# Kernel optimization log

Hardware: AMD Instinct MI355X
Metric: run time of the kernel (lower is better)

Reference implementation:

```python
import jax, jax.numpy as jnp
import numpy as np

NUM_HEADS = 16
LN_EPS = 1e-5


def _transpose_qkv(X, num_heads):
    # Faithful to the repo's (buggy) transpose_qkv:
    # (B,S,D) -> (B,S,H,D/H) -> permute (B,H,S,D/H) -> reshape (B,S,D)
    B, S, D = X.shape
    X = X.reshape(B, S, num_heads, D // num_heads)
    X = jnp.transpose(X, (0, 2, 1, 3))
    return X.reshape(B, S, D)


def _layer_norm(x, w, b):
    mu = jnp.mean(x, axis=-1, keepdims=True)
    var = jnp.var(x, axis=-1, keepdims=True)
    return (x - mu) * jax.lax.rsqrt(var + LN_EPS) * w + b


def setup_inputs() -> dict:
    key = jax.random.key(0)
    ks = jax.random.split(key, 4)
    B, S, D = 4, 2048, 1024
    scale = 1.0 / np.sqrt(D)
    return {
        "src": jax.random.normal(ks[0], (B, S, D), dtype=jnp.float32),
        "W_q": jax.random.normal(ks[1], (D, D), dtype=jnp.float32) * scale,
        "W_k": jax.random.normal(ks[2], (D, D), dtype=jnp.float32) * scale,
        "W_v": jax.random.normal(ks[3], (D, D), dtype=jnp.float32) * scale,
        "ln1_w": jnp.ones((D,), dtype=jnp.float32),
        "ln1_b": jnp.zeros((D,), dtype=jnp.float32),
        "ln2_w": jnp.ones((D,), dtype=jnp.float32),
        "ln2_b": jnp.zeros((D,), dtype=jnp.float32),
    }


def reference(src, W_q, W_k, W_v, ln1_w, ln1_b, ln2_w, ln2_b):
    # W_* stored as (in, out): y = x @ W  (equivalent to torch Linear, bias=False)
    q = _transpose_qkv(src @ W_q, NUM_HEADS)  # (B,S,D)
    k = _transpose_qkv(src @ W_k, NUM_HEADS)
    v = _transpose_qkv(src @ W_v, NUM_HEADS)
    d = q.shape[-1]  # note: full hidden dim, per the buggy transpose_qkv
    scores = jnp.einsum("bqd,bkd->bqk", q, k) / jnp.sqrt(jnp.float32(d))
    a = jax.nn.softmax(scores, axis=-1)          # (B,S,S) attention weights
    att = jnp.einsum("bqk,bkd->bqd", a, v)       # (B,S,D)
    src2 = _layer_norm(att, ln1_w, ln1_b)        # norm1
    X = _layer_norm(src + src2, ln2_w, ln2_b)    # AddNorm (dropout=0 in eval)
    return (X, a)
```

## Files before the change

### kernel.cpp

```cpp
#include <hip/hip_runtime.h>

typedef _Float16 f16;
typedef __attribute__((ext_vector_type(2))) _Float16 f16x2;
typedef __attribute__((ext_vector_type(4))) _Float16 f16x4;
typedef __attribute__((ext_vector_type(8))) _Float16 f16x8;
typedef __attribute__((ext_vector_type(4))) float f32x4;

#define D_MODEL 1024
#define SEQ 2048
#define NBATCH 4
#define NROWS (NBATCH * SEQ)

__device__ __forceinline__ void gload16(const void* g, void* l) {
  __builtin_amdgcn_global_load_lds(
      (__attribute__((address_space(1))) void*)(void*)g,
      (__attribute__((address_space(3))) void*)l, 16, 0, 0);
}

#define BARF                                   \
  do {                                         \
    asm volatile("" ::: "memory");             \
    __builtin_amdgcn_s_barrier();              \
    asm volatile("" ::: "memory");             \
  } while (0)
#define LGK asm volatile("s_waitcnt lgkmcnt(0)" ::: "memory")
#define LGK8 asm volatile("s_waitcnt lgkmcnt(8)" ::: "memory")
#define PRIO1 __builtin_amdgcn_s_setprio(1)
#define PRIO0 __builtin_amdgcn_s_setprio(0)


#define STAGE_A(D, H)                                        \
  {                                                          \
    f16* d_ = lds + ((D) * 2 + (H)) * 8192 + t * 8;          \
    gload16((H) ? aP2 : aP0, d_);                            \
    gload16((H) ? aP3 : aP1, d_ + 4096);                     \
  }
#define STAGE_B(D, H)                                        \
  {                                                          \
    if constexpr (BN == 256) {                               \
      f16* d_ = lds + 32768 + ((D) * 2 + (H)) * 8192 + t * 8;\
      gload16((H) ? bP2 : bP0, d_);                          \
      gload16((H) ? bP3 : bP1, d_ + 4096);                   \
    } else {                                                 \
      f16* d_ = lds + 32768 + (D) * 8192 + t * 8;            \
      gload16(bP0, d_);                                      \
      gload16(bP1, d_ + 4096);                               \
    }                                                        \
  }
#define ADVA                                                 \
  {                                                          \
    if (ka < NT - 1) {                                       \
      ka++;                                                  \
      aP0 += stepA; aP1 += stepA; aP2 += stepA; aP3 += stepA;\
    }                                                        \
  }
#define ADVB                                                 \
  {                                                          \
    if (kb < NT - 1) {                                       \
      kb++;                                                  \
      bP0 += stepB; bP1 += stepB;                            \
      if constexpr (BN == 256) { bP2 += stepB; bP3 += stepB; } \
    }                                                        \
  }
#define VMC_STEADY                                           \
  {                                                          \
    if constexpr (BN == 256) {                               \
      asm volatile("s_waitcnt vmcnt(4)" ::: "memory");       \
    } else {                                                 \
      asm volatile("s_waitcnt vmcnt(2)" ::: "memory");       \
    }                                                        \
  }
#define RD_A(D, MH)                                          \
  _Pragma("unroll") for (int mi = 0; mi < 4; ++mi)           \
  _Pragma("unroll") for (int kh = 0; kh < 2; ++kh) {         \
    const int rr = (MH) * 64 + mi * 16 + fr;                 \
    fa[mi][kh] = *(const f16x8*)(lds + ((D) * 2 + wm) * 8192 \
        + rr * 64 + (((g0 + kh * 4) ^ (rr & 7)) << 3));      \
  }
#define RD_B(D, NH)                                          \
  _Pragma("unroll") for (int j = 0; j < NJ; ++j)             \
  _Pragma("unroll") for (int kh = 0; kh < 2; ++kh) {         \
    int rbr, base;                                           \
    if constexpr (BN == 256) {                               \
      rbr = (wn & 1) * 64 + fr * 4 + (NH) * 2 + j;           \
      base = 32768 + ((D) * 2 + (wn >> 1)) * 8192;           \
    } else {                                                 \
      rbr = wn * 32 + fr * 2 + (NH);                         \
      base = 32768 + (D) * 8192;                             \
    }                                                        \
    fb[NH][j][kh] = *(const f16x8*)(lds + base + rbr * 64 +  \
        (((g0 + kh * 4) ^ ((rbr >> 2) & 7)) << 3));          \
  }
#define MFMA_Q(MH, NH)                                       \
  _Pragma("unroll") for (int mi = 0; mi < 4; ++mi)           \
  _Pragma("unroll") for (int j = 0; j < NJ; ++j)             \
  _Pragma("unroll") for (int kh = 0; kh < 2; ++kh)           \
    acc[((MH) * 4 + mi) * 2 * NJ + (NH) * NJ + j] =          \
        __builtin_amdgcn_mfma_f32_16x16x32_f16(              \
            fa[mi][kh], fb[NH][j][kh],                       \
            acc[((MH) * 4 + mi) * 2 * NJ + (NH) * NJ + j], 0, 0, 0);

template <int BN>
__device__ __forceinline__ void gemm8p(
    const f16* aP0, const f16* aP1, const f16* aP2, const f16* aP3,
    const f16* bP0, const f16* bP1, const f16* bP2, const f16* bP3,
    int stepA, int stepB, int NT, f16* lds, f32x4* acc)
{
  constexpr int NJ = BN / 128;
  const int t = threadIdx.x, l = t & 63;
  const int w = t >> 6, wm = w >> 2, wn = w & 3;
  const int fr = l & 15, g0 = l >> 4;
  f16x8 fa[4][2], fb[2][NJ][2];
#pragma unroll
  for (int i = 0; i < 8 * 2 * NJ; ++i) acc[i] = f32x4{0.f, 0.f, 0.f, 0.f};
  int ka = 0, kb = 0;
  (void)bP2; (void)bP3;

  STAGE_A(0, 0); STAGE_A(0, 1); ADVA;
  if constexpr (BN == 256) { STAGE_B(0, 0); STAGE_B(0, 1); }
  else { STAGE_B(0, 0); }
  ADVB;
  if constexpr (BN == 256) { STAGE_B(1, 0); STAGE_B(1, 1); }
  else { STAGE_B(1, 0); }
  ADVB;
  VMC_STEADY;
  BARF;

#pragma unroll 1
  for (int it = 0; it < NT / 2; ++it) {
    RD_A(0, 0); RD_B(0, 0);
    STAGE_A(1, 0);
    LGK8;
    BARF; LGK;
    PRIO1; MFMA_Q(0, 0); PRIO0;
    BARF;
    RD_B(0, 1);
    STAGE_A(1, 1); ADVA;
    BARF; LGK;
    PRIO1; MFMA_Q(0, 1); PRIO0;
    BARF;
    RD_A(0, 1);
    STAGE_B(0, 0);
    if constexpr (BN == 128) ADVB;
    BARF; LGK;
    PRIO1; MFMA_Q(1, 0); PRIO0;
    BARF;
    if constexpr (BN == 256) { STAGE_B(0, 1); ADVB; }
    VMC_STEADY;
    BARF;
    PRIO1; MFMA_Q(1, 1); PRIO0;
    BARF;
    RD_A(1, 0); RD_B(1, 0);
    STAGE_A(0, 0);
    LGK8;
    BARF; LGK;
    PRIO1; MFMA_Q(0, 0); PRIO0;
    BARF;
    RD_B(1, 1);
    STAGE_A(0, 1); ADVA;
    BARF; LGK;
    PRIO1; MFMA_Q(0, 1); PRIO0;
    BARF;
    RD_A(1, 1);
    STAGE_B(1, 0);
    if constexpr (BN == 128) ADVB;
    BARF; LGK;
    PRIO1; MFMA_Q(1, 0); PRIO0;
    BARF;
    if constexpr (BN == 256) { STAGE_B(1, 1); ADVB; }
    VMC_STEADY;
    BARF;
    PRIO1; MFMA_Q(1, 1); PRIO0;
    BARF;
  }
}

__global__ __launch_bounds__(512, 2) void k_qkv3(
    const f16* __restrict__ srch, const f16* __restrict__ wt,
    f16* __restrict__ qp, f16* __restrict__ kp, f16* __restrict__ vp)
{
  __shared__ f16 lds[65536];
  const int t = threadIdx.x, l = t & 63;
  const int w = t >> 6, wm = w >> 2, wn = w & 3;
  const int fr = l & 15, g0 = l >> 4, c = t & 7;
  const int bid = blockIdx.x;
  const int sb = (bid & 7) * 48 + (bid >> 3);
  const int bx = sb & 31, by = sb >> 5;
  const int z = by >> 2, cb = by & 3;
  const f16 *aP[4], *bP[4];
#pragma unroll
  for (int i = 0; i < 4; ++i) {
    const int rl = i * 64 + (t >> 3);
    aP[i] = srch + (size_t)(bx * 256 + rl) * 1024 + ((c ^ (rl & 7)) << 3);
    bP[i] = wt + ((size_t)z << 20) + (size_t)(cb * 256 + rl) * 1024 +
            ((c ^ ((rl >> 2) & 7)) << 3);
  }
  f32x4 acc[32];
  gemm8p<256>(aP[0], aP[1], aP[2], aP[3], bP[0], bP[1], bP[2], bP[3],
              64, 64, 16, lds, acc);
  f16* dst = (z == 0) ? qp : (z == 1 ? kp : vp);
  const int col = cb * 256 + wn * 64 + fr * 4;
#pragma unroll
  for (int mi = 0; mi < 8; ++mi)
#pragma unroll
    for (int q = 0; q < 4; ++q) {
      const int row = bx * 256 + wm * 128 + mi * 16 + g0 * 4 + q;
      f16x4 o = {(f16)acc[mi * 4 + 0][q], (f16)acc[mi * 4 + 1][q],
                 (f16)acc[mi * 4 + 2][q], (f16)acc[mi * 4 + 3][q]};
      *(f16x4*)(dst + (size_t)row * 1024 + col) = o;
    }
}

__global__ __launch_bounds__(512, 2) void k_scores(
    const f16* __restrict__ qp, const f16* __restrict__ kp,
    f16* __restrict__ abf)
{
  __shared__ f16 lds[65536];
  const int t = threadIdx.x, l = t & 63;
  const int w = t >> 6, wm = w >> 2, wn = w & 3;
  const int fr = l & 15, g0 = l >> 4, c = t & 7;
  const int b = blockIdx.z;
  const f16* qb = qp + ((size_t)b << 21);
  const f16* kb = kp + ((size_t)b << 21);
  const f16 *aP[4], *bP[4];
#pragma unroll
  for (int i = 0; i < 4; ++i) {
    const int rl = i * 64 + (t >> 3);
    const int spA = blockIdx.x * 256 + rl;
    aP[i] = qb + (size_t)((spA & 127) << 4) * 1024 + ((spA >> 7) << 6) +
            ((c ^ (rl & 7)) << 3);
    const int spB = blockIdx.y * 256 + rl;
    bP[i] = kb + (size_t)((spB & 127) << 4) * 1024 + ((spB >> 7) << 6) +
            ((c ^ ((rl >> 2) & 7)) << 3);
  }
  f32x4 acc[32];
  gemm8p<256>(aP[0], aP[1], aP[2], aP[3], bP[0], bP[1], bP[2], bP[3],
              1024, 1024, 16, lds, acc);
  f16* Cb = abf + ((size_t)b << 22);
  const int col = blockIdx.y * 256 + wn * 64 + fr * 4;
#pragma unroll
  for (int mi = 0; mi < 8; ++mi)
#pragma unroll
    for (int q = 0; q < 4; ++q) {
      const int row = blockIdx.x * 256 + wm * 128 + mi * 16 + g0 * 4 + q;
      f16x4 o = {(f16)(acc[mi * 4 + 0][q] * 0.03125f),
                 (f16)(acc[mi * 4 + 1][q] * 0.03125f),
                 (f16)(acc[mi * 4 + 2][q] * 0.03125f),
                 (f16)(acc[mi * 4 + 3][q] * 0.03125f)};
      *(f16x4*)(Cb + (size_t)row * 2048 + col) = o;
    }
}

__global__ __launch_bounds__(512, 2) void k_att(
    const f16* __restrict__ abf, const f16* __restrict__ vtT,
    f16* __restrict__ attb)
{
  __shared__ f16 lds[49152];
  const int t = threadIdx.x, l = t & 63;
  const int w = t >> 6, wm = w >> 2, wn = w & 3;
  const int fr = l & 15, g0 = l >> 4, c = t & 7;
  const int b = blockIdx.z;
  const f16* ab = abf + ((size_t)b << 22);
  const f16* vb = vtT + ((size_t)b << 21);
  const f16 *aP[4], *bP[2];
#pragma unroll
  for (int i = 0; i < 4; ++i) {
    const int rl = i * 64 + (t >> 3);
    aP[i] = ab + (size_t)(blockIdx.x * 256 + rl) * 2048 + ((c ^ (rl & 7)) << 3);
  }
#pragma unroll
  for (int i = 0; i < 2; ++i) {
    const int rl = i * 64 + (t >> 3);
    bP[i] = vb + (size_t)(blockIdx.y * 128 + rl) * 2048 +
            ((c ^ ((rl >> 2) & 7)) << 3);
  }
  f32x4 acc[16];
  gemm8p<128>(aP[0], aP[1], aP[2], aP[3], bP[0], bP[1], bP[0], bP[0],
              64, 64, 32, lds, acc);
  f16* Cb = attb + ((size_t)b << 21);
  const int col = blockIdx.y * 128 + wn * 32 + fr * 2;
#pragma unroll
  for (int mi = 0; mi < 8; ++mi)
#pragma unroll
    for (int q = 0; q < 4; ++q) {
      const int row = blockIdx.x * 256 + wm * 128 + mi * 16 + g0 * 4 + q;
      f16x2 o = {(f16)acc[mi * 2 + 0][q], (f16)acc[mi * 2 + 1][q]};
      *(f16x2*)(Cb + (size_t)row * 1024 + col) = o;
    }
}

__global__ __launch_bounds__(256) void k_prep(
    const float* __restrict__ src, const float* __restrict__ w0,
    const float* __restrict__ w1, const float* __restrict__ w2,
    f16* __restrict__ srch, f16* __restrict__ wt)
{
  const int b = blockIdx.x, t = threadIdx.x;
  if (b < 4096) {
    const size_t i = (size_t)b * 256 + t;
    const float4* p = (const float4*)src;
    float4 v0 = p[2 * i], v1 = p[2 * i + 1];
    f16x8 o;
    o[0] = (f16)v0.x; o[1] = (f16)v0.y; o[2] = (f16)v0.z; o[3] = (f16)v0.w;
    o[4] = (f16)v1.x; o[5] = (f16)v1.y; o[6] = (f16)v1.z; o[7] = (f16)v1.w;
    *(f16x8*)(srch + 8 * i) = o;
    return;
  }
  const int id = b - 4096;
  const int z = id >> 8, rem = id & 255;
  const int bx = rem & 15, by = rem >> 4;
  const float* in = (z == 0) ? w0 : (z == 1 ? w1 : w2);
  f16* o = wt + ((size_t)z << 20);
  __shared__ f16 tile[64][65];
  const int rr = t >> 4, c4 = (t & 15) * 4;
  const int r0 = bx * 64, c0 = by * 64;
#pragma unroll
  for (int i = 0; i < 4; ++i) {
    float4 f = *(const float4*)(in + (size_t)(r0 + rr + 16 * i) * 1024 + c0 + c4);
    tile[rr + 16 * i][c4 + 0] = (f16)f.x;
    tile[rr + 16 * i][c4 + 1] = (f16)f.y;
    tile[rr + 16 * i][c4 + 2] = (f16)f.z;
    tile[rr + 16 * i][c4 + 3] = (f16)f.w;
  }
  __syncthreads();
#pragma unroll
  for (int i = 0; i < 4; ++i) {
    const int n = c0 + rr + 16 * i;
    f16* dst = o + (size_t)n * 1024 + r0 + c4;
    dst[0] = tile[c4 + 0][rr + 16 * i];
    dst[1] = tile[c4 + 1][rr + 16 * i];
    dst[2] = tile[c4 + 2][rr + 16 * i];
    dst[3] = tile[c4 + 3][rr + 16 * i];
  }
}

__global__ __launch_bounds__(256) void k_softscr(
    float* __restrict__ out, f16* __restrict__ abf,
    const f16* __restrict__ vp, f16* __restrict__ vtT)
{
  __shared__ f16 shm[64][68];
  const int t = threadIdx.x;
  if (blockIdx.x < 8192) {
    float* red = (float*)&shm[0][0];
    const size_t base = (size_t)blockIdx.x * 2048;
    const int lane = t & 63, w = t >> 6;
    f16x8 v = *(const f16x8*)(abf + base + (size_t)t * 8);
    float x[8];
#pragma unroll
    for (int j = 0; j < 8; ++j) x[j] = (float)v[j];
    float m = fmaxf(fmaxf(fmaxf(x[0], x[1]), fmaxf(x[2], x[3])),
                    fmaxf(fmaxf(x[4], x[5]), fmaxf(x[6], x[7])));
#pragma unroll
    for (int off = 1; off < 64; off <<= 1) m = fmaxf(m, __shfl_xor(m, off));
    if (lane == 0) red[w] = m;
    __syncthreads();
    m = fmaxf(fmaxf(red[0], red[1]), fmaxf(red[2], red[3]));
    float s = 0.f;
#pragma unroll
    for (int j = 0; j < 8; ++j) { x[j] = __expf(x[j] - m); s += x[j]; }
#pragma unroll
    for (int off = 1; off < 64; off <<= 1) s += __shfl_xor(s, off);
    if (lane == 0) red[4 + w] = s;
    __syncthreads();
    s = red[4] + red[5] + red[6] + red[7];
    const float inv = 1.0f / s;
#pragma unroll
    for (int j = 0; j < 8; ++j) x[j] *= inv;
    float4 o0 = {x[0], x[1], x[2], x[3]}, o1 = {x[4], x[5], x[6], x[7]};
    ((float4*)(out + base))[2 * t] = o0;
    ((float4*)(out + base))[2 * t + 1] = o1;
    f16x8 ov;
#pragma unroll
    for (int j = 0; j < 8; ++j) ov[j] = (f16)x[j];
    *(f16x8*)(abf + base + (size_t)t * 8) = ov;
    return;
  }
  const int id = blockIdx.x - 8192;
  const int sx = id & 31, sy = (id >> 5) & 15, bz = id >> 9;
  const int sp0 = sx * 64, dp0 = sy * 64;
  const int d6 = dp0 >> 6;
  const int jb = (sp0 >> 7) << 6;
  const int sbase = sp0 & 127;
  const f16* srcv = vp + ((size_t)bz << 21);
  f16* dstv = vtT + ((size_t)bz << 21);
#pragma unroll
  for (int p = 0; p < 2; ++p) {
    const int u = p * 32 + (t >> 3);
    const int s = ((sbase + u) << 4) | d6;
    const int cc = (t & 7) << 3;
    f16x8 v = *(const f16x8*)(srcv + (size_t)s * 1024 + jb + cc);
    *(f16x4*)&shm[u][cc]     = f16x4{v[0], v[1], v[2], v[3]};
    *(f16x4*)&shm[u][cc + 4] = f16x4{v[4], v[5], v[6], v[7]};
  }
  __syncthreads();
#pragma unroll
  for (int p = 0; p < 2; ++p) {
    const int cc = p * 32 + (t >> 3);
    const int v0 = (t & 7) << 3;
    f16x8 o;
#pragma unroll
    for (int j = 0; j < 8; ++j) o[j] = shm[v0 + j][cc];
    *(f16x8*)(dstv + (size_t)(dp0 + cc) * 2048 + sp0 + v0) = o;
  }
}

__global__ __launch_bounds__(256) void k_ln(
    const f16* __restrict__ attb, const float* __restrict__ src,
    const float* __restrict__ w1, const float* __restrict__ b1,
    const float* __restrict__ w2, const float* __restrict__ b2,
    float* __restrict__ out)
{
  const size_t base = (size_t)blockIdx.x * 1024;
  const int t = threadIdx.x, lane = t & 63, w = t >> 6;
  f16x4 a4 = ((const f16x4*)(attb + base))[t];
  float ax = (float)a4[0], ay = (float)a4[1], az = (float)a4[2], aw = (float)a4[3];
  float s = ax + ay + az + aw;
  float s2 = ax * ax + ay * ay + az * az + aw * aw;
#pragma unroll
  for (int off = 1; off < 64; off <<= 1) {
    s += __shfl_xor(s, off);
    s2 += __shfl_xor(s2, off);
  }
  __shared__ float red[16];
  if (lane == 0) { red[w] = s; red[4 + w] = s2; }
  __syncthreads();
  s = red[0] + red[1] + red[2] + red[3];
  s2 = red[4] + red[5] + red[6] + red[7];
  float mu = s * (1.0f / 1024.0f);
  float var = s2 * (1.0f / 1024.0f) - mu * mu;
  float rs = rsqrtf(var + 1e-5f);
  float4 W1 = ((const float4*)w1)[t], B1 = ((const float4*)b1)[t];
  float4 sv = ((const float4*)(src + base))[t];
  float y0 = sv.x + (ax - mu) * rs * W1.x + B1.x;
  float y1 = sv.y + (ay - mu) * rs * W1.y + B1.y;
  float y2 = sv.z + (az - mu) * rs * W1.z + B1.z;
  float y3 = sv.w + (aw - mu) * rs * W1.w + B1.w;
  s = y0 + y1 + y2 + y3;
  s2 = y0 * y0 + y1 * y1 + y2 * y2 + y3 * y3;
#pragma unroll
  for (int off = 1; off < 64; off <<= 1) {
    s += __shfl_xor(s, off);
    s2 += __shfl_xor(s2, off);
  }
  if (lane == 0) { red[8 + w] = s; red[12 + w] = s2; }
  __syncthreads();
  s = red[8] + red[9] + red[10] + red[11];
  s2 = red[12] + red[13] + red[14] + red[15];
  mu = s * (1.0f / 1024.0f);
  var = s2 * (1.0f / 1024.0f) - mu * mu;
  rs = rsqrtf(var + 1e-5f);
  float4 W2 = ((const float4*)w2)[t], B2 = ((const float4*)b2)[t];
  float4 o;
  o.x = (y0 - mu) * rs * W2.x + B2.x;
  o.y = (y1 - mu) * rs * W2.y + B2.y;
  o.z = (y2 - mu) * rs * W2.z + B2.z;
  o.w = (y3 - mu) * rs * W2.w + B2.w;
  ((float4*)(out + base))[t] = o;
}

extern "C" void kernel_launch(void* const* d_in, const int* in_sizes, int n_in,
                              void* d_out, int out_size, void* d_ws, size_t ws_size,
                              hipStream_t stream) {
  const float* src = (const float*)d_in[0];
  const float* Wq  = (const float*)d_in[1];
  const float* Wk  = (const float*)d_in[2];
  const float* Wv  = (const float*)d_in[3];
  const float* l1w = (const float*)d_in[4];
  const float* l1b = (const float*)d_in[5];
  const float* l2w = (const float*)d_in[6];
  const float* l2b = (const float*)d_in[7];
  float* Xout = (float*)d_out;
  float* Aout = Xout + (size_t)NROWS * D_MODEL;

  char* ws = (char*)d_ws;
  f16* srch = (f16*)ws;
  f16* wt   = (f16*)(ws + (16u << 20));
  f16* qp   = (f16*)(ws + (22u << 20));
  f16* kp   = (f16*)(ws + (38u << 20));
  f16* vp   = (f16*)(ws + (54u << 20));
  f16* vtT  = (f16*)(ws + (70u << 20));
  f16* abf  = (f16*)(ws + (86u << 20));
  f16* attb = (f16*)(ws + (118u << 20));

  k_prep<<<4864, 256, 0, stream>>>(src, Wq, Wk, Wv, srch, wt);
  k_qkv3<<<384, 512, 0, stream>>>(srch, wt, qp, kp, vp);
  k_scores<<<dim3(8, 8, 4), 512, 0, stream>>>(qp, kp, abf);
  k_softscr<<<8192 + 2048, 256, 0, stream>>>(Aout, abf, vp, vtT);
  k_att<<<dim3(8, 8, 4), 512, 0, stream>>>(abf, vtT, attb);
  k_ln<<<NROWS, 256, 0, stream>>>(attb, src, l1w, l1b, l2w, l2b, Xout);
}
```

Before: 201.2 us.

## Switch GEMM core to 32x32x16 MFMA with simplified double-buffered pipeline

Replaces the 16x16x32 MFMA GEMM core with 32x32x16 MFMA tiles. The new core uses a simpler two-phase-per-k-tile schedule with fewer barriers and drops the explicit lgkmcnt waits. LDS swizzles and B-operand addressing change to match the new fragment layout. The QKV kernel loses its blockIdx swizzle for L2 locality and moves to a 2D grid. Epilogues now store single f16 scalars instead of vector stores, which adds store instructions and gives less coalesced writes.

```diff
diff --git a/kernel.cpp b/kernel.cpp
--- a/kernel.cpp
+++ b/kernel.cpp
@@ -1,10 +1,9 @@
 #include <hip/hip_runtime.h>
 
 typedef _Float16 f16;
-typedef __attribute__((ext_vector_type(2))) _Float16 f16x2;
 typedef __attribute__((ext_vector_type(4))) _Float16 f16x4;
 typedef __attribute__((ext_vector_type(8))) _Float16 f16x8;
-typedef __attribute__((ext_vector_type(4))) float f32x4;
+typedef __attribute__((ext_vector_type(16))) float f32x16;
 
 #define D_MODEL 1024
 #define SEQ 2048
@@ -23,154 +22,120 @@
     __builtin_amdgcn_s_barrier();              \
     asm volatile("" ::: "memory");             \
   } while (0)
-#define LGK asm volatile("s_waitcnt lgkmcnt(0)" ::: "memory")
-#define LGK8 asm volatile("s_waitcnt lgkmcnt(8)" ::: "memory")
 #define PRIO1 __builtin_amdgcn_s_setprio(1)
 #define PRIO0 __builtin_amdgcn_s_setprio(0)
 
-
-#define STAGE_A(D, H)                                        \
-  {                                                          \
-    f16* d_ = lds + ((D) * 2 + (H)) * 8192 + t * 8;          \
-    gload16((H) ? aP2 : aP0, d_);                            \
-    gload16((H) ? aP3 : aP1, d_ + 4096);                     \
-  }
-#define STAGE_B(D, H)                                        \
-  {                                                          \
-    if constexpr (BN == 256) {                               \
-      f16* d_ = lds + 32768 + ((D) * 2 + (H)) * 8192 + t * 8;\
-      gload16((H) ? bP2 : bP0, d_);                          \
-      gload16((H) ? bP3 : bP1, d_ + 4096);                   \
-    } else {                                                 \
-      f16* d_ = lds + 32768 + (D) * 8192 + t * 8;            \
-      gload16(bP0, d_);                                      \
-      gload16(bP1, d_ + 4096);                               \
-    }                                                        \
-  }
-#define ADVA                                                 \
-  {                                                          \
-    if (ka < NT - 1) {                                       \
-      ka++;                                                  \
-      aP0 += stepA; aP1 += stepA; aP2 += stepA; aP3 += stepA;\
-    }                                                        \
-  }
-#define ADVB                                                 \
-  {                                                          \
-    if (kb < NT - 1) {                                       \
-      kb++;                                                  \
-      bP0 += stepB; bP1 += stepB;                            \
-      if constexpr (BN == 256) { bP2 += stepB; bP3 += stepB; } \
-    }                                                        \
-  }
-#define VMC_STEADY                                           \
-  {                                                          \
-    if constexpr (BN == 256) {                               \
-      asm volatile("s_waitcnt vmcnt(4)" ::: "memory");       \
-    } else {                                                 \
-      asm volatile("s_waitcnt vmcnt(2)" ::: "memory");       \
-    }                                                        \
-  }
-#define RD_A(D, MH)                                          \
-  _Pragma("unroll") for (int mi = 0; mi < 4; ++mi)           \
-  _Pragma("unroll") for (int kh = 0; kh < 2; ++kh) {         \
-    const int rr = (MH) * 64 + mi * 16 + fr;                 \
-    fa[mi][kh] = *(const f16x8*)(lds + ((D) * 2 + wm) * 8192 \
-        + rr * 64 + (((g0 + kh * 4) ^ (rr & 7)) << 3));      \
-  }
-#define RD_B(D, NH)                                          \
-  _Pragma("unroll") for (int j = 0; j < NJ; ++j)             \
-  _Pragma("unroll") for (int kh = 0; kh < 2; ++kh) {         \
-    int rbr, base;                                           \
-    if constexpr (BN == 256) {                               \
-      rbr = (wn & 1) * 64 + fr * 4 + (NH) * 2 + j;           \
-      base = 32768 + ((D) * 2 + (wn >> 1)) * 8192;           \
-    } else {                                                 \
-      rbr = wn * 32 + fr * 2 + (NH);                         \
-      base = 32768 + (D) * 8192;                             \
-    }                                                        \
-    fb[NH][j][kh] = *(const f16x8*)(lds + base + rbr * 64 +  \
-        (((g0 + kh * 4) ^ ((rbr >> 2) & 7)) << 3));          \
-  }
-#define MFMA_Q(MH, NH)                                       \
-  _Pragma("unroll") for (int mi = 0; mi < 4; ++mi)           \
-  _Pragma("unroll") for (int j = 0; j < NJ; ++j)             \
-  _Pragma("unroll") for (int kh = 0; kh < 2; ++kh)           \
-    acc[((MH) * 4 + mi) * 2 * NJ + (NH) * NJ + j] =          \
-        __builtin_amdgcn_mfma_f32_16x16x32_f16(              \
-            fa[mi][kh], fb[NH][j][kh],                       \
-            acc[((MH) * 4 + mi) * 2 * NJ + (NH) * NJ + j], 0, 0, 0);
+#define ADVA                                                      \
+  {                                                               \
+    if (ka < NT - 1) {                                            \
+      ka++;                                                       \
+      aP0 += stepA; aP1 += stepA; aP2 += stepA; aP3 += stepA;     \
+    }                                                             \
+  }
+#define ADVB                                                      \
+  {                                                               \
+    if (kb < NT - 1) {                                            \
+      kb++;                                                       \
+      bP0 += stepB; bP1 += stepB;                                 \
+      if constexpr (BN == 256) { bP2 += stepB; bP3 += stepB; }    \
+    }                                                             \
+  }
+#define STA(SL, H)                                                \
+  {                                                               \
+    f16* d_ = lds + ((SL) * 2 + (H)) * 8192 + t * 8;              \
+    gload16((H) ? aP2 : aP0, d_);                                 \
+    gload16((H) ? aP3 : aP1, d_ + 4096);                          \
+  }
+#define STB_ALL(SL)                                               \
+  {                                                               \
+    if constexpr (BN == 256) {                                    \
+      f16* d0_ = lds + 32768 + ((SL) * 2 + 0) * 8192 + t * 8;     \
+      gload16(bP0, d0_);                                          \
+      gload16(bP1, d0_ + 4096);                                   \
+      f16* d1_ = lds + 32768 + ((SL) * 2 + 1) * 8192 + t * 8;     \
+      gload16(bP2, d1_);                                          \
+      gload16(bP3, d1_ + 4096);                                   \
+    } else {                                                      \
+      f16* d_ = lds + 32768 + (SL) * 8192 + t * 8;                \
+      gload16(bP0, d_);                                           \
+      gload16(bP1, d_ + 4096);                                    \
+    }                                                             \
+  }
+#define VMC                                                       \
+  {                                                               \
+    if constexpr (BN == 256) {                                    \
+      asm volatile("s_waitcnt vmcnt(4)" ::: "memory");            \
+    } else {                                                      \
+      asm volatile("s_waitcnt vmcnt(2)" ::: "memory");            \
+    }                                                             \
+  }
+#define RDA(D, G)                                                 \
+  _Pragma("unroll") for (int mf = 0; mf < 2; ++mf)                \
+  _Pragma("unroll") for (int ks = 0; ks < 4; ++ks) {              \
+    const int rr = ((G) * 2 + mf) * 32 + l31;                     \
+    fa[mf][ks] = *(const f16x8*)(lds + ((D) * 2 + wm) * 8192 +    \
+        rr * 64 + ((((ks << 1) | hi) ^ (rr & 7)) << 3));          \
+  }
+#define RDB(D)                                                    \
+  _Pragma("unroll") for (int nf = 0; nf < NF; ++nf)               \
+  _Pragma("unroll") for (int ks = 0; ks < 4; ++ks) {              \
+    const int rb = wn * (BN / 4) + nf * 32 + l31;                 \
+    int base_, rl_;                                               \
+    if constexpr (BN == 256) {                                    \
+      base_ = 32768 + ((D) * 2 + (rb >> 7)) * 8192;               \
+      rl_ = rb & 127;                                             \
+    } else {                                                      \
+      base_ = 32768 + (D) * 8192;                                 \
+      rl_ = rb;                                                   \
+    }                                                             \
+    fb[nf][ks] = *(const f16x8*)(lds + base_ + rl_ * 64 +         \
+        ((((ks << 1) | hi) ^ (rb & 7)) << 3));                    \
+  }
+#define MFG(G)                                                    \
+  _Pragma("unroll") for (int ks = 0; ks < 4; ++ks)                \
+  _Pragma("unroll") for (int mf = 0; mf < 2; ++mf)                \
+  _Pragma("unroll") for (int nf = 0; nf < NF; ++nf)               \
+    acc[((G) * 2 + mf) * NF + nf] =                               \
+        __builtin_amdgcn_mfma_f32_32x32x16_f16(                   \
+            fa[mf][ks], fb[nf][ks], acc[((G) * 2 + mf) * NF + nf],\
+            0, 0, 0);
 
 template <int BN>
-__device__ __forceinline__ void gemm8p(
+__device__ __forceinline__ void gemm32(
     const f16* aP0, const f16* aP1, const f16* aP2, const f16* aP3,
     const f16* bP0, const f16* bP1, const f16* bP2, const f16* bP3,
-    int stepA, int stepB, int NT, f16* lds, f32x4* acc)
-{
-  constexpr int NJ = BN / 128;
+    int stepA, int stepB, int NT, f16* lds, f32x16* acc)
+{
+  constexpr int NF = BN / 128;
   const int t = threadIdx.x, l = t & 63;
   const int w = t >> 6, wm = w >> 2, wn = w & 3;
-  const int fr = l & 15, g0 = l >> 4;
-  f16x8 fa[4][2], fb[2][NJ][2];
-#pragma unroll
-  for (int i = 0; i < 8 * 2 * NJ; ++i) acc[i] = f32x4{0.f, 0.f, 0.f, 0.f};
+  const int l31 = l & 31, hi = l >> 5;
+  f16x8 fa[2][4], fb[NF][4];
+  f32x16 zz;
+#pragma unroll
+  for (int j = 0; j < 16; ++j) zz[j] = 0.f;
+#pragma unroll
+  for (int i = 0; i < 4 * NF; ++i) acc[i] = zz;
   int ka = 0, kb = 0;
   (void)bP2; (void)bP3;
 
-  STAGE_A(0, 0); STAGE_A(0, 1); ADVA;
-  if constexpr (BN == 256) { STAGE_B(0, 0); STAGE_B(0, 1); }
-  else { STAGE_B(0, 0); }
-  ADVB;
-  if constexpr (BN == 256) { STAGE_B(1, 0); STAGE_B(1, 1); }
-  else { STAGE_B(1, 0); }
-  ADVB;
-  VMC_STEADY;
+  STA(0, 0); STA(0, 1); ADVA;
+  STB_ALL(0); ADVB;
+  STB_ALL(1); ADVB;
+  VMC;
   BARF;
 
 #pragma unroll 1
-  for (int it = 0; it < NT / 2; ++it) {
-    RD_A(0, 0); RD_B(0, 0);
-    STAGE_A(1, 0);
-    LGK8;
-    BARF; LGK;
-    PRIO1; MFMA_Q(0, 0); PRIO0;
+  for (int kt = 0; kt < NT; ++kt) {
+    const int sl = kt & 1;
+    STA(sl ^ 1, 0); STA(sl ^ 1, 1); ADVA;
+    RDA(sl, 0); RDB(sl);
+    PRIO1; MFG(0); PRIO0;
     BARF;
-    RD_B(0, 1);
-    STAGE_A(1, 1); ADVA;
-    BARF; LGK;
-    PRIO1; MFMA_Q(0, 1); PRIO0;
-    BARF;
-    RD_A(0, 1);
-    STAGE_B(0, 0);
-    if constexpr (BN == 128) ADVB;
-    BARF; LGK;
-    PRIO1; MFMA_Q(1, 0); PRIO0;
-    BARF;
-    if constexpr (BN == 256) { STAGE_B(0, 1); ADVB; }
-    VMC_STEADY;
-    BARF;
-    PRIO1; MFMA_Q(1, 1); PRIO0;
-    BARF;
-    RD_A(1, 0); RD_B(1, 0);
-    STAGE_A(0, 0);
-    LGK8;
-    BARF; LGK;
-    PRIO1; MFMA_Q(0, 0); PRIO0;
-    BARF;
-    RD_B(1, 1);
-    STAGE_A(0, 1); ADVA;
-    BARF; LGK;
-    PRIO1; MFMA_Q(0, 1); PRIO0;
-    BARF;
-    RD_A(1, 1);
-    STAGE_B(1, 0);
-    if constexpr (BN == 128) ADVB;
-    BARF; LGK;
-    PRIO1; MFMA_Q(1, 0); PRIO0;
-    BARF;
-    if constexpr (BN == 256) { STAGE_B(1, 1); ADVB; }
-    VMC_STEADY;
-    BARF;
-    PRIO1; MFMA_Q(1, 1); PRIO0;
+    RDA(sl, 1);
+    STB_ALL(sl); ADVB;
+    VMC;
+    PRIO1; MFG(1); PRIO0;
     BARF;
   }
 }
@@ -182,10 +147,8 @@
   __shared__ f16 lds[65536];
   const int t = threadIdx.x, l = t & 63;
   const int w = t >> 6, wm = w >> 2, wn = w & 3;
-  const int fr = l & 15, g0 = l >> 4, c = t & 7;
-  const int bid = blockIdx.x;
-  const int sb = (bid & 7) * 48 + (bid >> 3);
-  const int bx = sb & 31, by = sb >> 5;
+  const int l31 = l & 31, hi = l >> 5, c = t & 7;
+  const int bx = blockIdx.x, by = blockIdx.y;
   const int z = by >> 2, cb = by & 3;
   const f16 *aP[4], *bP[4];
 #pragma unroll
@@ -193,21 +156,23 @@
     const int rl = i * 64 + (t >> 3);
     aP[i] = srch + (size_t)(bx * 256 + rl) * 1024 + ((c ^ (rl & 7)) << 3);
     bP[i] = wt + ((size_t)z << 20) + (size_t)(cb * 256 + rl) * 1024 +
-            ((c ^ ((rl >> 2) & 7)) << 3);
-  }
-  f32x4 acc[32];
-  gemm8p<256>(aP[0], aP[1], aP[2], aP[3], bP[0], bP[1], bP[2], bP[3],
+            ((c ^ (rl & 7)) << 3);
+  }
+  f32x16 acc[8];
+  gemm32<256>(aP[0], aP[1], aP[2], aP[3], bP[0], bP[1], bP[2], bP[3],
               64, 64, 16, lds, acc);
   f16* dst = (z == 0) ? qp : (z == 1 ? kp : vp);
-  const int col = cb * 256 + wn * 64 + fr * 4;
-#pragma unroll
-  for (int mi = 0; mi < 8; ++mi)
-#pragma unroll
-    for (int q = 0; q < 4; ++q) {
-      const int row = bx * 256 + wm * 128 + mi * 16 + g0 * 4 + q;
-      f16x4 o = {(f16)acc[mi * 4 + 0][q], (f16)acc[mi * 4 + 1][q],
-                 (f16)acc[mi * 4 + 2][q], (f16)acc[mi * 4 + 3][q]};
-      *(f16x4*)(dst + (size_t)row * 1024 + col) = o;
+  const int rbase = bx * 256 + wm * 128 + 4 * hi;
+#pragma unroll
+  for (int mf = 0; mf < 4; ++mf)
+#pragma unroll
+    for (int nf = 0; nf < 2; ++nf) {
+      const int col = cb * 256 + wn * 64 + nf * 32 + l31;
+#pragma unroll
+      for (int r = 0; r < 16; ++r) {
+        const int row = rbase + mf * 32 + (r & 3) + 8 * (r >> 2);
+        dst[(size_t)row * 1024 + col] = (f16)acc[mf * 2 + nf][r];
+      }
     }
 }
 
@@ -218,7 +183,7 @@
   __shared__ f16 lds[65536];
   const int t = threadIdx.x, l = t & 63;
   const int w = t >> 6, wm = w >> 2, wn = w & 3;
-  const int fr = l & 15, g0 = l >> 4, c = t & 7;
+  const int l31 = l & 31, hi = l >> 5, c = t & 7;
   const int b = blockIdx.z;
   const f16* qb = qp + ((size_t)b << 21);
   const f16* kb = kp + ((size_t)b << 21);
@@ -231,23 +196,23 @@
             ((c ^ (rl & 7)) << 3);
     const int spB = blockIdx.y * 256 + rl;
     bP[i] = kb + (size_t)((spB & 127) << 4) * 1024 + ((spB >> 7) << 6) +
-            ((c ^ ((rl >> 2) & 7)) << 3);
-  }
-  f32x4 acc[32];
-  gemm8p<256>(aP[0], aP[1], aP[2], aP[3], bP[0], bP[1], bP[2], bP[3],
+            ((c ^ (rl & 7)) << 3);
+  }
+  f32x16 acc[8];
+  gemm32<256>(aP[0], aP[1], aP[2], aP[3], bP[0], bP[1], bP[2], bP[3],
               1024, 1024, 16, lds, acc);
   f16* Cb = abf + ((size_t)b << 22);
-  const int col = blockIdx.y * 256 + wn * 64 + fr * 4;
-#pragma unroll
-  for (int mi = 0; mi < 8; ++mi)
-#pragma unroll
-    for (int q = 0; q < 4; ++q) {
-      const int row = blockIdx.x * 256 + wm * 128 + mi * 16 + g0 * 4 + q;
-      f16x4 o = {(f16)(acc[mi * 4 + 0][q] * 0.03125f),
-                 (f16)(acc[mi * 4 + 1][q] * 0.03125f),
-                 (f16)(acc[mi * 4 + 2][q] * 0.03125f),
-                 (f16)(acc[mi * 4 + 3][q] * 0.03125f)};
-      *(f16x4*)(Cb + (size_t)row * 2048 + col) = o;
+  const int rbase = blockIdx.x * 256 + wm * 128 + 4 * hi;
+#pragma unroll
+  for (int mf = 0; mf < 4; ++mf)
+#pragma unroll
+    for (int nf = 0; nf < 2; ++nf) {
+      const int col = blockIdx.y * 256 + wn * 64 + nf * 32 + l31;
+#pragma unroll
+      for (int r = 0; r < 16; ++r) {
+        const int row = rbase + mf * 32 + (r & 3) + 8 * (r >> 2);
+        Cb[(size_t)row * 2048 + col] = (f16)(acc[mf * 2 + nf][r] * 0.03125f);
+      }
     }
 }
 
@@ -258,7 +223,7 @@
   __shared__ f16 lds[49152];
   const int t = threadIdx.x, l = t & 63;
   const int w = t >> 6, wm = w >> 2, wn = w & 3;
-  const int fr = l & 15, g0 = l >> 4, c = t & 7;
+  const int l31 = l & 31, hi = l >> 5, c = t & 7;
   const int b = blockIdx.z;
   const f16* ab = abf + ((size_t)b << 22);
   const f16* vb = vtT + ((size_t)b << 21);
@@ -272,20 +237,20 @@
   for (int i = 0; i < 2; ++i) {
     const int rl = i * 64 + (t >> 3);
     bP[i] = vb + (size_t)(blockIdx.y * 128 + rl) * 2048 +
-            ((c ^ ((rl >> 2) & 7)) << 3);
-  }
-  f32x4 acc[16];
-  gemm8p<128>(aP[0], aP[1], aP[2], aP[3], bP[0], bP[1], bP[0], bP[0],
+            ((c ^ (rl & 7)) << 3);
+  }
+  f32x16 acc[4];
+  gemm32<128>(aP[0], aP[1], aP[2], aP[3], bP[0], bP[1], bP[0], bP[0],
               64, 64, 32, lds, acc);
   f16* Cb = attb + ((size_t)b << 21);
-  const int col = blockIdx.y * 128 + wn * 32 + fr * 2;
-#pragma unroll
-  for (int mi = 0; mi < 8; ++mi)
-#pragma unroll
-    for (int q = 0; q < 4; ++q) {
-      const int row = blockIdx.x * 256 + wm * 128 + mi * 16 + g0 * 4 + q;
-      f16x2 o = {(f16)acc[mi * 2 + 0][q], (f16)acc[mi * 2 + 1][q]};
-      *(f16x2*)(Cb + (size_t)row * 1024 + col) = o;
+  const int rbase = blockIdx.x * 256 + wm * 128 + 4 * hi;
+  const int col = blockIdx.y * 128 + wn * 32 + l31;
+#pragma unroll
+  for (int mf = 0; mf < 4; ++mf)
+#pragma unroll
+    for (int r = 0; r < 16; ++r) {
+      const int row = rbase + mf * 32 + (r & 3) + 8 * (r >> 2);
+      Cb[(size_t)row * 1024 + col] = (f16)acc[mf][r];
     }
 }
 
@@ -482,7 +447,7 @@
   f16* attb = (f16*)(ws + (118u << 20));
 
   k_prep<<<4864, 256, 0, stream>>>(src, Wq, Wk, Wv, srch, wt);
-  k_qkv3<<<384, 512, 0, stream>>>(srch, wt, qp, kp, vp);
+  k_qkv3<<<dim3(32, 12), 512, 0, stream>>>(srch, wt, qp, kp, vp);
   k_scores<<<dim3(8, 8, 4), 512, 0, stream>>>(qp, kp, abf);
   k_softscr<<<8192 + 2048, 256, 0, stream>>>(Aout, abf, vp, vtT);
   k_att<<<dim3(8, 8, 4), 512, 0, stream>>>(abf, vtT, attb);
```

Measured after the change: 217.3 us. 1.08x slower.
